# Performance work log

Hardware: AMD Instinct MI355X
Metric: run time of the kernel (lower is better)

Reference implementation:

```python
import jax, jax.numpy as jnp
import numpy as np

DIM = 512
HEADS = 8
DH = DIM // HEADS          # 64, dim_head = dim // 8
M = DIM // 2               # 256 landmarks
ITERS = 6                  # pinv iterations
KS = 33                    # residual depthwise conv kernel (lucidrains default)
N_LAYERS = 2
LN_EPS = 1e-5


def layer_norm(x, scale, bias):
    mu = x.mean(-1, keepdims=True)
    var = ((x - mu) ** 2).mean(-1, keepdims=True)
    return (x - mu) * jax.lax.rsqrt(var + LN_EPS) * scale + bias


def sinusoidal_pe(T, d, dtype):
    pos = np.arange(T)[:, None]
    div = np.exp(np.arange(0, d, 2) * (-np.log(10000.0) / d))
    pe = np.zeros((T, d), dtype=np.float32)
    pe[:, 0::2] = np.sin(pos * div)
    pe[:, 1::2] = np.cos(pos * div)
    return jnp.asarray(pe, dtype=dtype)


def iter_pinv(x):
    # Newton-Schulz Moore-Penrose iteration (lucidrains), global-max scaling
    ax = jnp.abs(x)
    denom = ax.sum(-1).max() * ax.sum(-2).max()
    z = jnp.swapaxes(x, -1, -2) / denom
    I = jnp.eye(x.shape[-1], dtype=x.dtype)
    for _ in range(ITERS):
        xz = x @ z
        z = 0.25 * (z @ (13.0 * I - xz @ (15.0 * I - xz @ (7.0 * I - xz))))
    return z


def nystrom_attention(x, qkv_w, out_w, out_b, conv_w):
    b, n, d = x.shape
    pad = (-n) % M                       # left-pad so seq divisible by M
    xp = jnp.pad(x, ((0, 0), (pad, 0), (0, 0)))
    N = n + pad
    q, k, v = [t.reshape(b, N, HEADS, DH).transpose(0, 2, 1, 3)
               for t in jnp.split(xp @ qkv_w, 3, axis=-1)]  # each [b,h,N,dh]
    q = q * (DH ** -0.5)
    l = N // M                           # segment length per landmark
    q_l = q.reshape(b, HEADS, M, l, DH).mean(3)   # [b,h,M,dh]
    k_l = k.reshape(b, HEADS, M, l, DH).mean(3)
    attn1 = jax.nn.softmax(jnp.einsum('bhid,bhjd->bhij', q, k_l), -1)    # [b,h,N,M]
    attn2 = jax.nn.softmax(jnp.einsum('bhid,bhjd->bhij', q_l, k_l), -1)  # [b,h,M,M]
    attn3 = jax.nn.softmax(jnp.einsum('bhid,bhjd->bhij', q_l, k), -1)    # [b,h,M,N]
    out = attn1 @ (iter_pinv(attn2) @ (attn3 @ v))                       # [b,h,N,dh]
    # residual depthwise conv over sequence, per head (groups=heads)
    P = KS // 2
    out = out + jax.lax.conv_general_dilated(
        v, conv_w, (1, 1), ((P, P), (0, 0)),
        dimension_numbers=('NCHW', 'OIHW', 'NCHW'), feature_group_count=HEADS)
    out = out.transpose(0, 2, 1, 3).reshape(b, N, d)
    out = out @ out_w + out_b
    return out[:, -n:]


def setup_inputs() -> dict:
    key = jax.random.key(0)
    ks = jax.random.split(key, 12)
    B, T, IN_DIM = 4, 4095, 1024
    s = 0.02
    return {
        'data': jax.random.normal(ks[0], (B, T, IN_DIM), jnp.float32),
        'fc1_w': jax.random.normal(ks[1], (IN_DIM, DIM), jnp.float32) * s,
        'fc1_b': jnp.zeros((DIM,), jnp.float32),
        'cls_token': jax.random.normal(ks[2], (1, 1, DIM), jnp.float32),
        'ln_scale': jnp.ones((N_LAYERS, DIM), jnp.float32),
        'ln_bias': jnp.zeros((N_LAYERS, DIM), jnp.float32),
        'qkv_w': jax.random.normal(ks[3], (N_LAYERS, DIM, 3 * DIM), jnp.float32) * s,
        'out_w': jax.random.normal(ks[4], (N_LAYERS, DIM, DIM), jnp.float32) * s,
        'out_b': jnp.zeros((N_LAYERS, DIM), jnp.float32),
        'conv_w': jax.random.normal(ks[5], (N_LAYERS, HEADS, 1, KS, 1), jnp.float32) * s,
        'fnorm_scale': jnp.ones((DIM,), jnp.float32),
        'fnorm_bias': jnp.zeros((DIM,), jnp.float32),
        'fcout_w': jax.random.normal(ks[6], (DIM, 1), jnp.float32) * s,
        'fcout_b': jnp.zeros((1,), jnp.float32),
    }


def reference(data, fc1_w, fc1_b, cls_token, ln_scale, ln_bias, qkv_w, out_w,
              out_b, conv_w, fnorm_scale, fnorm_bias, fcout_w, fcout_b):
    B, T, _ = data.shape
    h = jax.nn.relu(data @ fc1_w + fc1_b)
    h = h + sinusoidal_pe(T, DIM, h.dtype)
    cls = jnp.broadcast_to(cls_token, (B, 1, DIM))
    h = jnp.concatenate([cls, h], axis=1)
    for i in range(N_LAYERS):
        h = h + nystrom_attention(layer_norm(h, ln_scale[i], ln_bias[i]),
                                  qkv_w[i], out_w[i], out_b[i], conv_w[i])
    h = layer_norm(h, fnorm_scale, fnorm_bias)
    logits = (h[:, 0] @ fcout_w + fcout_b)[:, 0]
    y_prob = jax.nn.sigmoid(logits)
    y_hat = (y_prob > 0.5).astype(jnp.int32)
    return logits, y_prob, y_hat
```

## Files before the change

### kernel.cpp

```cpp
#include <hip/hip_runtime.h>
#include <math.h>

typedef long long ll;
typedef __attribute__((ext_vector_type(8))) short short8;
typedef __attribute__((ext_vector_type(4))) float f32x4;

#define NBATCH 4
#define TSEQ   4095
#define NTOK   4096
#define DMODEL 512
#define NHEAD  8
#define DHEAD  64
#define NLAND  256
#define INDIM  1024
#define KCONV  33
#define NBH    32
#define NSPLIT 8

__device__ __forceinline__ float bred(float* red, float v, int tid, int op){
  red[tid] = v; __syncthreads();
  for (int s = 128; s > 0; s >>= 1){
    if (tid < s) red[tid] = op ? fmaxf(red[tid], red[tid+s]) : (red[tid] + red[tid+s]);
    __syncthreads();
  }
  float r = red[0];
  __syncthreads();
  return r;
}

__device__ __forceinline__ short f2bf(float f){
  unsigned u = __float_as_uint(f);
  u += 0x7fff + ((u>>16)&1);
  return (short)(u>>16);
}
__device__ __forceinline__ float bf2f(short s){
  return __uint_as_float(((unsigned)(unsigned short)s) << 16);
}

__global__ __launch_bounds__(256) void pe_table_k(float* __restrict__ pe){
  int idx = blockIdx.x*256 + threadIdx.x;
  if (idx >= TSEQ*DMODEL) return;
  int c = idx & 511; int t = idx >> 9;
  const double NEG = -9.210340371976184 / 512.0;
  double div = exp((double)(c & ~1) * NEG);
  float ang = (float)((double)t * div);
  pe[idx] = (c & 1) ? cosf(ang) : sinf(ang);
}

__global__ __launch_bounds__(256) void pe_cls_add_k(float* __restrict__ hb, const float* __restrict__ cls,
                                                    const float* __restrict__ pe){
  ll idx = (ll)blockIdx.x*256 + threadIdx.x;
  int c = (int)(idx & 511);
  ll rn = idx >> 9;
  int n = (int)(rn & 4095);
  if (n == 0) hb[idx] = cls[c];
  else        hb[idx] += pe[(ll)(n-1)*512 + c];
}

__global__ __launch_bounds__(256) void cvt_bf16_k(const float* __restrict__ in, short* __restrict__ out, int n8){
  int idx = blockIdx.x*256 + threadIdx.x;
  for (int i = idx; i < n8; i += gridDim.x*256){
    const f32x4* p = (const f32x4*)(in + (ll)i*8);
    f32x4 a = p[0], b = p[1];
    short8 v;
    v[0]=f2bf(a[0]); v[1]=f2bf(a[1]); v[2]=f2bf(a[2]); v[3]=f2bf(a[3]);
    v[4]=f2bf(b[0]); v[5]=f2bf(b[1]); v[6]=f2bf(b[2]); v[7]=f2bf(b[3]);
    ((short8*)out)[i] = v;
  }
}

__global__ __launch_bounds__(256) void transpose_bf16_k(const float* __restrict__ in, short* __restrict__ out,
                                                        int K, int N, ll sIn, ll sOut){
  __shared__ float t[64][65];
  int L = blockIdx.z;
  in  += (ll)L*sIn;
  out += (ll)L*sOut;
  int n0 = blockIdx.x*64, k0 = blockIdx.y*64;
  int tid = threadIdx.x;
  for (int e = tid; e < 4096; e += 256){
    int r = e >> 6, c = e & 63;
    t[r][c] = in[(ll)(k0 + r)*N + n0 + c];
  }
  __syncthreads();
  for (int e = tid; e < 4096; e += 256){
    int r = e >> 6, c = e & 63;
    out[(ll)(n0 + r)*K + k0 + c] = f2bf(t[c][r]);
  }
}

__global__ __launch_bounds__(256) void ln_rows_k(const float* __restrict__ in, short* __restrict__ out,
                                                 const float* __restrict__ sc, const float* __restrict__ bi){
  __shared__ float red[256];
  ll row = blockIdx.x;
  const float* xr = in + row*DMODEL;
  short* orow = out + row*DMODEL;
  int tid = threadIdx.x;
  float v0 = xr[tid], v1 = xr[tid+256];
  float mu = bred(red, v0+v1, tid, 0) * (1.f/512.f);
  float d0 = v0-mu, d1 = v1-mu;
  float var = bred(red, d0*d0 + d1*d1, tid, 0) * (1.f/512.f);
  float inv = 1.f / sqrtf(var + 1e-5f);
  orow[tid]     = f2bf(d0*inv*sc[tid]     + bi[tid]);
  orow[tid+256] = f2bf(d1*inv*sc[tid+256] + bi[tid+256]);
}

template<int BM, int BN, int AB, int BMODE, int CB, int SW>
__global__ __launch_bounds__(256)
void mgemm(const void* __restrict__ Av, const void* __restrict__ Bv,
           void* __restrict__ Cv, const void* __restrict__ Ev,
           const float* __restrict__ bias,
           int Mr, int K, int lda, int ldb, int ldc,
           ll sA, ll sB, ll sC,
           float c0, float c1, int flags)
{
  constexpr int MI = BM/32, NJ = BN/32;
  __shared__ __align__(16) short As[BM*64];
  __shared__ __align__(16) short Bs[BN*64];
  int z = blockIdx.z;
  int bx = blockIdx.x, by = blockIdx.y;
  if (SW){
    int nwg = gridDim.x*gridDim.y;
    int lin = by*gridDim.x + bx;
    int q = nwg >> 3, r = nwg & 7;
    int xcd = lin & 7, idx = lin >> 3;
    int wg = (xcd < r) ? (xcd*(q+1) + idx) : (r*(q+1) + (xcd - r)*q + idx);
    bx = wg % gridDim.x; by = wg / gridDim.x;
  }
  int n0 = bx*BN, m0 = by*BM;
  int tid = threadIdx.x;
  int lane = tid & 63, w = tid >> 6;
  int wr = w >> 1, wc = w & 1;
  int l15 = lane & 15, l4 = lane >> 4;

  f32x4 acc[MI][NJ];
  #pragma unroll
  for (int i = 0; i < MI; i++)
    #pragma unroll
    for (int j = 0; j < NJ; j++) acc[i][j] = (f32x4){0.f,0.f,0.f,0.f};

  for (int k0 = 0; k0 < K; k0 += 64){
    #pragma unroll
    for (int it = 0; it < BM/32; ++it){
      int tau = tid + 256*it;
      int row = tau >> 3, slot = tau & 7;
      int grow = m0 + row;
      short8 v;
      if (AB){
        if (grow < Mr) v = *(const short8*)((const short*)Av + (ll)z*sA + (ll)grow*lda + k0 + slot*8);
        else v = (short8){0,0,0,0,0,0,0,0};
      } else {
        f32x4 p0 = {0.f,0.f,0.f,0.f}, p1 = {0.f,0.f,0.f,0.f};
        if (grow < Mr){
          const float* ap = (const float*)Av + (ll)z*sA + (ll)grow*lda + k0 + slot*8;
          p0 = *(const f32x4*)ap; p1 = *(const f32x4*)(ap+4);
        }
        v[0]=f2bf(p0[0]); v[1]=f2bf(p0[1]); v[2]=f2bf(p0[2]); v[3]=f2bf(p0[3]);
        v[4]=f2bf(p1[0]); v[5]=f2bf(p1[1]); v[6]=f2bf(p1[2]); v[7]=f2bf(p1[3]);
      }
      ((short8*)As)[row*8 + (slot ^ (row&7))] = v;
    }
    #pragma unroll
    for (int it = 0; it < BN/32; ++it){
      int tau = tid + 256*it;
      if (BMODE == 2){
        int n = tau >> 3, slot = tau & 7;
        short8 v = *(const short8*)((const short*)Bv + (ll)z*sB + (ll)(n0 + n)*ldb + k0 + slot*8);
        ((short8*)Bs)[n*8 + (slot ^ (n&7))] = v;
      } else {
        int n = tau & (BN-1), slot = tau >> (BN==128 ? 7 : 6);
        short8 v;
        if (BMODE == 1){
          const short* bp = (const short*)Bv + (ll)z*sB + (ll)(k0 + slot*8)*ldb + n0 + n;
          #pragma unroll
          for (int i = 0; i < 8; i++) v[i] = bp[(ll)i*ldb];
        } else {
          const float* bp = (const float*)Bv + (ll)z*sB + (ll)(k0 + slot*8)*ldb + n0 + n;
          #pragma unroll
          for (int i = 0; i < 8; i++) v[i] = f2bf(bp[(ll)i*ldb]);
        }
        ((short8*)Bs)[n*8 + (slot ^ (n&7))] = v;
      }
    }
    __syncthreads();
    #pragma unroll
    for (int kc = 0; kc < 2; kc++){
      short8 af[MI], bfr[NJ];
      #pragma unroll
      for (int i = 0; i < MI; i++){
        int row = wr*(BM/2) + i*16 + l15;
        int g = kc*4 + l4;
        af[i] = ((short8*)As)[row*8 + (g ^ (row&7))];
      }
      #pragma unroll
      for (int j = 0; j < NJ; j++){
        int col = wc*(BN/2) + j*16 + l15;
        int g = kc*4 + l4;
        bfr[j] = ((short8*)Bs)[col*8 + (g ^ (col&7))];
      }
      #pragma unroll
      for (int i = 0; i < MI; i++)
        #pragma unroll
        for (int j = 0; j < NJ; j++)
          acc[i][j] = __builtin_amdgcn_mfma_f32_16x16x32_bf16(af[i], bfr[j], acc[i][j], 0, 0, 0);
    }
    __syncthreads();
  }

  #pragma unroll
  for (int i = 0; i < MI; i++){
    int rbase = m0 + wr*(BM/2) + i*16 + l4*4;
    #pragma unroll
    for (int j = 0; j < NJ; j++){
      int col = n0 + wc*(BN/2) + j*16 + l15;
      #pragma unroll
      for (int r = 0; r < 4; r++){
        int m = rbase + r;
        if (m >= Mr) continue;
        float v = acc[i][j][r];
        if (flags & 4){
          float ev = CB ? bf2f(((const short*)Ev + (ll)z*sC)[(ll)m*ldc + col])
                        : ((const float*)Ev + (ll)z*sC)[(ll)m*ldc + col];
          v = c0 * ev + c1 * v;
        }
        if (flags & 1) v += bias[col];
        if (flags & 2) v = fmaxf(v, 0.f);
        int om = (flags & 16) ? (m + m/TSEQ + 1) : m;
        ll ci = (ll)z*sC + (ll)om*ldc + col;
        if (CB){
          short* Cs = (short*)Cv;
          if (flags & 8) v += bf2f(Cs[ci]);
          Cs[ci] = f2bf(v);
        } else {
          float* Cf = (float*)Cv;
          if (flags & 8) v += Cf[ci];
          Cf[ci] = v;
        }
      }
    }
  }
}

__global__ __launch_bounds__(256)
void gemm_nt(const short* __restrict__ A, const short* __restrict__ Bm, float* __restrict__ C,
             int lda, int ldb, int ldc,
             ll sAb, ll sAh, ll sBb, ll sBh, ll sCb, ll sCh,
             float alpha)
{
  __shared__ float As[64][65];
  __shared__ float Bs[64][65];
  int z = blockIdx.z; int b = z >> 3; int h = z & 7;
  A  += (ll)b*sAb + (ll)h*sAh;
  Bm += (ll)b*sBb + (ll)h*sBh;
  C  += (ll)b*sCb + (ll)h*sCh;
  int n0 = blockIdx.x*64, m0 = blockIdx.y*64;
  int tid = threadIdx.x;
  int kk = tid & 63, rr = tid >> 6;
  #pragma unroll
  for (int r = 0; r < 16; r++){
    As[rr + 4*r][kk] = bf2f(A [(ll)(m0 + rr + 4*r)*lda + kk]);
    Bs[rr + 4*r][kk] = bf2f(Bm[(ll)(n0 + rr + 4*r)*ldb + kk]);
  }
  __syncthreads();
  int tx = tid & 15, ty = tid >> 4;
  float acc[4][4] = {};
  for (int k = 0; k < 64; k++){
    float a[4], bv[4];
    #pragma unroll
    for (int i = 0; i < 4; i++) a[i] = As[ty + 16*i][k];
    #pragma unroll
    for (int j = 0; j < 4; j++) bv[j] = Bs[tx + 16*j][k];
    #pragma unroll
    for (int i = 0; i < 4; i++)
      #pragma unroll
      for (int j = 0; j < 4; j++)
        acc[i][j] += a[i]*bv[j];
  }
  #pragma unroll
  for (int i = 0; i < 4; i++)
    #pragma unroll
    for (int j = 0; j < 4; j++)
      C[(ll)(m0 + ty + 16*i)*ldc + n0 + tx + 16*j] = alpha * acc[i][j];
}

__global__ __launch_bounds__(256)
void mflash_k(const short* __restrict__ Q, const short* __restrict__ K,
              const short* __restrict__ V, short* __restrict__ O,
              int ldq, int ldk, int ldv, int ldo, int nkeys, float alpha,
              ll sQb, ll sQh, ll sKb, ll sKh, ll sVb, ll sVh, ll sOb, ll sOh)
{
  __shared__ __align__(16) short Qs[64*64];
  __shared__ __align__(16) short Ks[64*64];
  __shared__ __align__(16) short Vs[64*64];
  __shared__ __align__(16) short Ps[64*64];
  __shared__ float Sl[64][68];
  __shared__ float m_l[64], s_l[64], scl[64];
  int z = blockIdx.z; int b = z >> 3; int h = z & 7;
  Q += (ll)b*sQb + (ll)h*sQh;
  K += (ll)b*sKb + (ll)h*sKh;
  V += (ll)b*sVb + (ll)h*sVh;
  O += (ll)b*sOb + (ll)h*sOh;
  int m0 = blockIdx.x*64;
  int tid = threadIdx.x;
  int lane = tid & 63, w = tid >> 6;
  int l15 = lane & 15, l4 = lane >> 4;
  int wr = w >> 1, wc = w & 1;

  #pragma unroll
  for (int it = 0; it < 2; it++){
    int tau = tid + 256*it;
    int row = tau >> 3, slot = tau & 7;
    short8 v = *(const short8*)(Q + (ll)(m0 + row)*ldq + slot*8);
    ((short8*)Qs)[row*8 + (slot ^ (row&7))] = v;
  }
  if (tid < 64){ m_l[tid] = -1e30f; s_l[tid] = 0.f; }
  f32x4 o[2][2];
  #pragma unroll
  for (int i = 0; i < 2; i++)
    #pragma unroll
    for (int j = 0; j < 2; j++) o[i][j] = (f32x4){0.f,0.f,0.f,0.f};

  for (int n0 = 0; n0 < nkeys; n0 += 64){
// ... 208 lines not shown
    for (int i = 0; i < 2; i++)
      #pragma unroll
      for (int j = 0; j < 2; j++)
        #pragma unroll
        for (int r = 0; r < 4; r++)
          Sl[wr*32 + i*16 + l4*4 + r][wc*32 + j*16 + l15] = s[i][j][r];
    __syncthreads();
    {
      int row = tid >> 2, q = tid & 3, cb = q*16;
      float sv[16];
      float cmax = -1e30f;
      #pragma unroll
      for (int cc = 0; cc < 16; cc++){ sv[cc] = Sl[row][cb+cc]; cmax = fmaxf(cmax, sv[cc]); }
      cmax = fmaxf(cmax, __shfl_xor(cmax, 1));
      cmax = fmaxf(cmax, __shfl_xor(cmax, 2));
      float mprev = m_l[row];
      float newm = fmaxf(mprev, cmax);
      float lsum = 0.f;
      short8 pv0, pv1;
      #pragma unroll
      for (int cc = 0; cc < 8; cc++){ float e = expf(sv[cc]-newm); lsum += e; pv0[cc] = f2bf(e); }
      #pragma unroll
      for (int cc = 0; cc < 8; cc++){ float e = expf(sv[8+cc]-newm); lsum += e; pv1[cc] = f2bf(e); }
      lsum += __shfl_xor(lsum, 1);
      lsum += __shfl_xor(lsum, 2);
      ((short8*)Ps)[row*8 + ((2*q)   ^ (row&7))] = pv0;
      ((short8*)Ps)[row*8 + ((2*q+1) ^ (row&7))] = pv1;
      if (q == 0){
        float scale = expf(mprev - newm);
        m_l[row] = newm;
        s_l[row] = s_l[row]*scale + lsum;
        scl[row] = scale;
      }
    }
    __syncthreads();
    #pragma unroll
    for (int i = 0; i < 2; i++)
      #pragma unroll
      for (int r = 0; r < 4; r++){
        float sc = scl[wr*32 + i*16 + l4*4 + r];
        #pragma unroll
        for (int j = 0; j < 2; j++) o[i][j][r] *= sc;
      }
    #pragma unroll
    for (int kc = 0; kc < 2; kc++){
      short8 ap[2], bv[2];
      int g = kc*4 + l4;
      #pragma unroll
      for (int i = 0; i < 2; i++){
        int row = wr*32 + i*16 + l15;
        ap[i] = ((short8*)Ps)[row*8 + (g ^ (row&7))];
      }
      #pragma unroll
      for (int j = 0; j < 2; j++){
        int d = wc*32 + j*16 + l15;
        bv[j] = ((short8*)Vs)[d*8 + (g ^ (d&7))];
      }
      #pragma unroll
      for (int i = 0; i < 2; i++)
        #pragma unroll
        for (int j = 0; j < 2; j++)
          o[i][j] = __builtin_amdgcn_mfma_f32_16x16x32_bf16(ap[i], bv[j], o[i][j], 0, 0, 0);
    }
  }
  int bs = z*NSPLIT + split;
  #pragma unroll
  for (int i = 0; i < 2; i++)
    #pragma unroll
    for (int j = 0; j < 2; j++)
      #pragma unroll
      for (int r = 0; r < 4; r++){
        int row = wr*32 + i*16 + l4*4 + r;
        int col = wc*32 + j*16 + l15;
        po[((ll)bs*NLAND + m0 + row)*64 + col] = o[i][j][r];
      }
  if (tid < 64){
    pm[(ll)bs*NLAND + m0 + tid] = m_l[tid];
    pl[(ll)bs*NLAND + m0 + tid] = s_l[tid];
  }
}

__global__ __launch_bounds__(256)
void flash3_comb_k(const float* __restrict__ po, const float* __restrict__ pm,
                   const float* __restrict__ pl, short* __restrict__ av){
  int bh = blockIdx.y;
  int row = blockIdx.x*4 + (threadIdx.x >> 6);
  int col = threadIdx.x & 63;
  float ms = -1e30f;
  float mv[NSPLIT];
  #pragma unroll
  for (int s = 0; s < NSPLIT; s++){
    mv[s] = pm[((ll)bh*NSPLIT + s)*NLAND + row];
    ms = fmaxf(ms, mv[s]);
  }
  float osum = 0.f, lsum = 0.f;
  #pragma unroll
  for (int s = 0; s < NSPLIT; s++){
    float wgt = expf(mv[s] - ms);
    osum += wgt * po[(((ll)bh*NSPLIT + s)*NLAND + row)*64 + col];
    lsum += wgt * pl[((ll)bh*NSPLIT + s)*NLAND + row];
  }
  av[((ll)bh*NLAND + row)*64 + col] = f2bf(osum / lsum);
}

__global__ __launch_bounds__(256) void softmax_rows_k(float* __restrict__ data, short* __restrict__ out16,
                                                      int cols){
  __shared__ float red[256];
  float* row = data + (ll)blockIdx.x * cols;
  short* row16 = out16 ? out16 + (ll)blockIdx.x * cols : nullptr;
  int tid = threadIdx.x;
  float m = -1e30f;
  for (int c = tid; c < cols; c += 256) m = fmaxf(m, row[c]);
  m = bred(red, m, tid, 1);
  float s = 0.f;
  for (int c = tid; c < cols; c += 256){ float e = expf(row[c] - m); row[c] = e; s += e; }
  s = bred(red, s, tid, 0);
  float inv = 1.f/s;
  for (int c = tid; c < cols; c += 256){
    float p = row[c] * inv;
    row[c] = p;
    if (row16) row16[c] = f2bf(p);
  }
}

__global__ __launch_bounds__(256) void landmarks_k(const short* __restrict__ qkv,
                                                   short* __restrict__ ql, short* __restrict__ kl){
  int idx = blockIdx.x*256 + threadIdx.x;
  int d = idx & 63;
  int i = (idx >> 6) & 255;
  int h = (idx >> 14) & 7;
  int b = idx >> 17;
  const short* base = qkv + ((ll)b*NTOK + (ll)i*16)*1536 + h*64 + d;
  float sq = 0.f, sk = 0.f;
  #pragma unroll
  for (int l = 0; l < 16; l++){ sq += bf2f(base[l*1536]); sk += bf2f(base[l*1536 + 512]); }
  ql[idx] = f2bf(sq * (0.125f/16.f));
  kl[idx] = f2bf(sk * (1.f/16.f));
}

__global__ void init_scal_k(unsigned* s){ s[0] = 0u; s[1] = 0u; }

__global__ __launch_bounds__(256) void a2_maxsums_k(const float* __restrict__ a2, unsigned* __restrict__ gm){
  __shared__ float red[256];
  const float* A = a2 + (ll)blockIdx.x*65536;
  int tid = threadIdx.x;
  float cs = 0.f, rs = 0.f;
  for (int i = 0; i < 256; i++) cs += A[i*256 + tid];
  for (int j = 0; j < 256; j++) rs += A[tid*256 + j];
  float cmax = bred(red, cs, tid, 1);
  float rmax = bred(red, rs, tid, 1);
  if (tid == 0){
    atomicMax(gm + 0, __float_as_uint(rmax));
    atomicMax(gm + 1, __float_as_uint(cmax));
  }
}

__global__ __launch_bounds__(256) void zinit_k(const float* __restrict__ a2, short* __restrict__ z,
                                               const unsigned* __restrict__ gm){
  float inv = 1.f / (__uint_as_float(gm[0]) * __uint_as_float(gm[1]));
  int idx = blockIdx.x*256 + threadIdx.x;
  int j = idx & 255, i = (idx >> 8) & 255, bh = idx >> 16;
  z[idx] = f2bf(a2[(ll)bh*65536 + j*256 + i] * inv);
}

__global__ __launch_bounds__(256) void dwconv_add_k(const short* __restrict__ qkv,
                                                    const float* __restrict__ cw, short* __restrict__ out){
  __shared__ float sv[160][64];
  __shared__ float w[KCONV];
  int z = blockIdx.y; int b = z >> 3; int h = z & 7;
  int t0 = blockIdx.x * 128;
  int tid = threadIdx.x;
  if (tid < KCONV) w[tid] = cw[h*KCONV + tid];
  const short* vbase = qkv + (ll)b*NTOK*1536 + 1024 + h*64;
  for (int e = tid; e < 160*64; e += 256){
    int r = e >> 6, d = e & 63;
    int t = t0 - 16 + r;
    sv[r][d] = (t >= 0 && t < NTOK) ? bf2f(vbase[(ll)t*1536 + d]) : 0.f;
  }
  __syncthreads();
  short* obase = out + (ll)b*NTOK*512 + h*64;
  for (int e = tid; e < 128*64; e += 256){
    int r = e >> 6, d = e & 63;
    float s = 0.f;
    #pragma unroll
    for (int kk = 0; kk < KCONV; kk++) s += sv[r+kk][d]*w[kk];
    ll oi = (ll)(t0+r)*512 + d;
    obase[oi] = f2bf(bf2f(obase[oi]) + s);
  }
}

__global__ __launch_bounds__(256) void head_k(const float* __restrict__ hb, const float* __restrict__ fns,
      const float* __restrict__ fnb, const float* __restrict__ fw, const float* __restrict__ fb,
      float* __restrict__ out){
  __shared__ float red[256];
  int b = blockIdx.x;
  const float* xr = hb + (ll)b*NTOK*DMODEL;
  int tid = threadIdx.x;
  float v0 = xr[tid], v1 = xr[tid+256];
  float mu = bred(red, v0+v1, tid, 0) * (1.f/512.f);
  float d0 = v0-mu, d1 = v1-mu;
  float var = bred(red, d0*d0 + d1*d1, tid, 0) * (1.f/512.f);
  float inv = 1.f/sqrtf(var + 1e-5f);
  float y0 = d0*inv*fns[tid]     + fnb[tid];
  float y1 = d1*inv*fns[tid+256] + fnb[tid+256];
  float dot = bred(red, y0*fw[tid] + y1*fw[tid+256], tid, 0);
  if (tid == 0){
    float logit = dot + fb[0];
    float prob = 1.f/(1.f + expf(-logit));
    out[b] = logit; out[4+b] = prob; out[8+b] = (prob > 0.5f) ? 1.f : 0.f;
  }
}

extern "C" void kernel_launch(void* const* d_in, const int* in_sizes, int n_in,
                              void* d_out, int out_size, void* d_ws, size_t ws_size,
                              hipStream_t stream)
{
  (void)in_sizes; (void)n_in; (void)out_size;
  const float* data  = (const float*)d_in[0];
  const float* fc1_w = (const float*)d_in[1];
  const float* fc1_b = (const float*)d_in[2];
  const float* cls   = (const float*)d_in[3];
  const float* ln_s  = (const float*)d_in[4];
  const float* ln_b  = (const float*)d_in[5];
  const float* qkv_w = (const float*)d_in[6];
  const float* out_w = (const float*)d_in[7];
  const float* out_b = (const float*)d_in[8];
  const float* convw = (const float*)d_in[9];
  const float* fns   = (const float*)d_in[10];
  const float* fnb   = (const float*)d_in[11];
  const float* fcw   = (const float*)d_in[12];
  const float* fcb   = (const float*)d_in[13];
  float* out = (float*)d_out;
  float* ws  = (float*)d_ws;

  float* h    = ws;
  short* xb   = (short*)(h + 8388608);
  short* qkvh = xb + 8388608;
  short* ql   = qkvh + 25165824;
  short* kl   = ql + 524288;
  float* a2f  = (float*)(kl + 524288);
  short* a2h  = (short*)(a2f + 2097152);
  short* zA   = a2h + 2097152;
  short* zB   = zA + 2097152;
  short* t1   = zB + 2097152;
  short* t2   = t1 + 2097152;
  short* t3   = t2 + 2097152;
  short* av   = t3 + 2097152;
  short* y2   = av + 524288;
  float* po   = (float*)(y2 + 524288);
  float* pm   = po + 4194304;
  float* pl   = pm + 65536;
  float* pe   = pl + 65536;
  short* datab = (short*)(pe + 2097152);
  short* fc1t  = datab + 16777216;
  short* qkvt  = fc1t + 524288;
  short* outt  = qkvt + 1572864;
  unsigned* scal = (unsigned*)(outt + 524288);

  const size_t NEED = (size_t)((char*)(scal + 2) - (char*)ws);
  if (ws_size < NEED) return;

  pe_table_k<<<(TSEQ*DMODEL + 255)/256, 256, 0, stream>>>(pe);
  cvt_bf16_k<<<2048, 256, 0, stream>>>(data, datab, (NBATCH*TSEQ*INDIM)/8);
  transpose_bf16_k<<<dim3(8, 16, 1), 256, 0, stream>>>(fc1_w, fc1t, INDIM, DMODEL, 0, 0);
  transpose_bf16_k<<<dim3(24, 8, 2), 256, 0, stream>>>(qkv_w, qkvt, DMODEL, 1536,
                                                       (ll)DMODEL*1536, (ll)1536*DMODEL);
  transpose_bf16_k<<<dim3(8, 8, 2), 256, 0, stream>>>(out_w, outt, DMODEL, DMODEL,
                                                      (ll)DMODEL*DMODEL, (ll)DMODEL*DMODEL);

  mgemm<128,128,1,2,0,1><<<dim3(4, 128, 1), 256, 0, stream>>>(
      datab, fc1t, h, nullptr, fc1_b,
      NBATCH*TSEQ, INDIM, INDIM, INDIM, DMODEL,
      0, 0, 0, 0.f, 0.f, 1|2|16);
  pe_cls_add_k<<<(NBATCH*NTOK*DMODEL)/256, 256, 0, stream>>>(h, cls, pe);

  for (int L = 0; L < 2; L++){
    const float* ob = out_b + (ll)L*DMODEL;
    const float* cw = convw + (ll)L*NHEAD*KCONV;
    const short* qwt = qkvt + (ll)L*1536*DMODEL;
    const short* owt = outt + (ll)L*DMODEL*DMODEL;

    ln_rows_k<<<NBATCH*NTOK, 256, 0, stream>>>(h, xb, ln_s + L*DMODEL, ln_b + L*DMODEL);
    mgemm<128,128,1,2,1,1><<<dim3(12, 128, 1), 256, 0, stream>>>(
        xb, qwt, qkvh, nullptr, nullptr,
        NBATCH*NTOK, DMODEL, DMODEL, DMODEL, 1536,
        0, 0, 0, 0.f, 0.f, 0);
    landmarks_k<<<2048, 256, 0, stream>>>(qkvh, ql, kl);

    gemm_nt<<<dim3(4, 4, NBH), 256, 0, stream>>>(
        ql, kl, a2f, 64, 64, 256,
        131072, 16384, 131072, 16384, 524288, 65536, 1.f);
    softmax_rows_k<<<NBH*NLAND, 256, 0, stream>>>(a2f, a2h, 256);

    init_scal_k<<<1, 1, 0, stream>>>(scal);
    a2_maxsums_k<<<NBH, 256, 0, stream>>>(a2f, scal);
    zinit_k<<<8192, 256, 0, stream>>>(a2f, zA, scal);

    short* zc = zA; short* zn = zB;
    for (int it = 0; it < 6; it++){
      mgemm<64,64,1,1,1,0><<<dim3(4, 4, NBH), 256, 0, stream>>>(
          a2h, zc, t1, nullptr, nullptr, 256, 256, 256, 256, 256,
          65536, 65536, 65536, 0.f, 0.f, 0);
      mgemm<64,64,1,1,1,0><<<dim3(4, 4, NBH), 256, 0, stream>>>(
          t1, t1, t2, t1, nullptr, 256, 256, 256, 256, 256,
          65536, 65536, 65536, 7.f, -1.f, 4);
      mgemm<64,64,1,1,1,0><<<dim3(4, 4, NBH), 256, 0, stream>>>(
          t1, t2, t3, t1, nullptr, 256, 256, 256, 256, 256,
          65536, 65536, 65536, 15.f, -1.f, 4);
      mgemm<64,64,1,1,1,0><<<dim3(4, 4, NBH), 256, 0, stream>>>(
          zc, t3, zn, zc, nullptr, 256, 256, 256, 256, 256,
          65536, 65536, 65536, 3.25f, -0.25f, 4);
      short* tmp = zc; zc = zn; zn = tmp;
    }

    mflash3_part_k<<<dim3(4, NSPLIT, NBH), 256, 0, stream>>>(
        ql, qkvh + 512, qkvh + 1024, po, pm, pl,
        64, 1536, 1536,
        131072, 16384, (ll)NTOK*1536, 64, (ll)NTOK*1536, 64);
    flash3_comb_k<<<dim3(64, NBH), 256, 0, stream>>>(po, pm, pl, av);

    mgemm<64,64,1,1,1,0><<<dim3(1, 4, NBH), 256, 0, stream>>>(
        zc, av, y2, nullptr, nullptr, 256, 256, 256, 64, 64,
        65536, 16384, 16384, 0.f, 0.f, 0);

    mflash_k<<<dim3(64, 1, NBH), 256, 0, stream>>>(
        qkvh, kl, y2, xb,
        1536, 64, 64, 512, NLAND, 0.125f,
        (ll)NTOK*1536, 64, 131072, 16384, 131072, 16384, (ll)NTOK*512, 64);

    dwconv_add_k<<<dim3(32, NBH), 256, 0, stream>>>(qkvh, cw, xb);

    mgemm<128,128,1,2,0,1><<<dim3(4, 128, 1), 256, 0, stream>>>(
        xb, owt, h, nullptr, ob,
        NBATCH*NTOK, DMODEL, DMODEL, DMODEL, DMODEL,
        0, 0, 0, 0.f, 0.f, 1|8);
  }

  head_k<<<4, 256, 0, stream>>>(h, fns, fnb, fcw, fcb, out);
}
```

Baseline: 1.308 ms.

## Fuse Newton-Schulz pinv chain into one cooperative kernel with grid syncs

Replaces the zinit kernel, the 24 small batched GEMM launches of the pseudo-inverse iteration and the final z@av GEMM with one cooperative kernel of 512 blocks. Each block owns a 64x64 tile of one head and uses grid.sync between dependent GEMM stages. The goal is to remove per-launch overhead and tail gaps across roughly 26 kernels per layer. The risks are the cost of the grid-wide barriers, a new and possibly slower inline GEMM tile with strided scalar B loads, and a fallback path if cooperative launch fails.

```diff
diff --git a/kernel.cpp b/kernel.cpp
--- a/kernel.cpp
+++ b/kernel.cpp
@@ -1,5 +1,8 @@
 #include <hip/hip_runtime.h>
+#include <hip/hip_cooperative_groups.h>
 #include <math.h>
+
+namespace cg = cooperative_groups;
 
 typedef long long ll;
 typedef __attribute__((ext_vector_type(8))) short short8;
@@ -237,6 +240,126 @@
         }
       }
     }
+  }
+}
+
+__device__ __forceinline__ void gtile(const short* __restrict__ A, int lda,
+                                      const short* __restrict__ B, int ldb,
+                                      short* __restrict__ C, int ldc,
+                                      const short* __restrict__ E, int lde,
+                                      int Kdim, float c0, float c1,
+                                      int m0, int n0, int tid,
+                                      short* As, short* Bs)
+{
+  int lane = tid & 63, w = tid >> 6;
+  int wr = w >> 1, wc = w & 1;
+  int l15 = lane & 15, l4 = lane >> 4;
+  f32x4 acc[2][2];
+  #pragma unroll
+  for (int i = 0; i < 2; i++)
+    #pragma unroll
+    for (int j = 0; j < 2; j++) acc[i][j] = (f32x4){0.f,0.f,0.f,0.f};
+
+  for (int k0 = 0; k0 < Kdim; k0 += 64){
+    __syncthreads();
+    #pragma unroll
+    for (int it = 0; it < 2; ++it){
+      int tau = tid + 256*it;
+      int row = tau >> 3, slot = tau & 7;
+      short8 v = *(const short8*)(A + (ll)(m0 + row)*lda + k0 + slot*8);
+      ((short8*)As)[row*8 + (slot ^ (row&7))] = v;
+    }
+    #pragma unroll
+    for (int it = 0; it < 2; ++it){
+      int tau = tid + 256*it;
+      int n = tau & 63, slot = tau >> 6;
+      const short* bp = B + (ll)(k0 + slot*8)*ldb + n0 + n;
+      short8 v;
+      #pragma unroll
+      for (int i = 0; i < 8; i++) v[i] = bp[(ll)i*ldb];
+      ((short8*)Bs)[n*8 + (slot ^ (n&7))] = v;
+    }
+    __syncthreads();
+    #pragma unroll
+    for (int kc = 0; kc < 2; kc++){
+      short8 af[2], bfr[2];
+      int g = kc*4 + l4;
+      #pragma unroll
+      for (int i = 0; i < 2; i++){
+        int row = i*16 + wr*32 + l15;
+        af[i] = ((short8*)As)[row*8 + (g ^ (row&7))];
+      }
+      #pragma unroll
+      for (int j = 0; j < 2; j++){
+        int col = j*16 + wc*32 + l15;
+        bfr[j] = ((short8*)Bs)[col*8 + (g ^ (col&7))];
+      }
+      #pragma unroll
+      for (int i = 0; i < 2; i++)
+        #pragma unroll
+        for (int j = 0; j < 2; j++)
+          acc[i][j] = __builtin_amdgcn_mfma_f32_16x16x32_bf16(af[i], bfr[j], acc[i][j], 0, 0, 0);
+    }
+  }
+  #pragma unroll
+  for (int i = 0; i < 2; i++)
+    #pragma unroll
+    for (int j = 0; j < 2; j++)
+      #pragma unroll
+      for (int r = 0; r < 4; r++){
+        int row = m0 + wr*32 + i*16 + l4*4 + r;
+        int col = n0 + wc*32 + j*16 + l15;
+        float v = c1 * acc[i][j][r];
+        if (E) v += c0 * bf2f(E[(ll)row*lde + col]);
+        C[(ll)row*ldc + col] = f2bf(v);
+      }
+}
+
+__global__ __launch_bounds__(256)
+void pinv_chain_k(const float* __restrict__ a2f, const short* __restrict__ a2h,
+                  short* __restrict__ zAg, short* __restrict__ zBg,
+                  short* __restrict__ t1g, short* __restrict__ t2g, short* __restrict__ t3g,
+                  const short* __restrict__ avg, short* __restrict__ y2g,
+                  const unsigned* __restrict__ gm)
+{
+  __shared__ __align__(16) short As[64*64];
+  __shared__ __align__(16) short Bs[64*64];
+  cg::grid_group grid = cg::this_grid();
+  int blk = blockIdx.x;
+  int bh = blk >> 4, tile = blk & 15;
+  int m0 = (tile >> 2)*64, n0 = (tile & 3)*64;
+  int tid = threadIdx.x;
+  const float* a2F = a2f + (ll)bh*65536;
+  const short* a2H = a2h + (ll)bh*65536;
+  short* zA = zAg + (ll)bh*65536;
+  short* zB = zBg + (ll)bh*65536;
+  short* t1 = t1g + (ll)bh*65536;
+  short* t2 = t2g + (ll)bh*65536;
+  short* t3 = t3g + (ll)bh*65536;
+
+  float inv = 1.f / (__uint_as_float(gm[0]) * __uint_as_float(gm[1]));
+  for (int e = tid; e < 4096; e += 256){
+    int r = e >> 6, c = e & 63;
+    zA[(ll)(m0 + r)*256 + n0 + c] = f2bf(a2F[(ll)(n0 + c)*256 + m0 + r] * inv);
+  }
+  grid.sync();
+
+  short* zc = zA; short* zn = zB;
+  for (int it = 0; it < 6; it++){
+    gtile(a2H, 256, zc, 256, t1, 256, nullptr, 256, 256, 0.f, 1.f, m0, n0, tid, As, Bs);
+    grid.sync();
+    gtile(t1, 256, t1, 256, t2, 256, t1, 256, 256, 7.f, -1.f, m0, n0, tid, As, Bs);
+    grid.sync();
+    gtile(t1, 256, t2, 256, t3, 256, t1, 256, 256, 15.f, -1.f, m0, n0, tid, As, Bs);
+    grid.sync();
+    gtile(zc, 256, t3, 256, zn, 256, zc, 256, 256, 3.25f, -0.25f, m0, n0, tid, As, Bs);
+    grid.sync();
+    short* tmp = zc; zc = zn; zn = tmp;
+  }
+  if ((tile & 3) == 0){
+    const short* av = avg + (ll)bh*16384;
+    short* y2 = y2g + (ll)bh*16384;
+    gtile(zc, 256, av, 64, y2, 64, nullptr, 64, 256, 0.f, 1.f, m0, 0, tid, As, Bs);
   }
 }
 
@@ -820,27 +943,8 @@
         ql, kl, a2f, 64, 64, 256,
         131072, 16384, 131072, 16384, 524288, 65536, 1.f);
     softmax_rows_k<<<NBH*NLAND, 256, 0, stream>>>(a2f, a2h, 256);
-
     init_scal_k<<<1, 1, 0, stream>>>(scal);
     a2_maxsums_k<<<NBH, 256, 0, stream>>>(a2f, scal);
-    zinit_k<<<8192, 256, 0, stream>>>(a2f, zA, scal);
-
-    short* zc = zA; short* zn = zB;
-    for (int it = 0; it < 6; it++){
-      mgemm<64,64,1,1,1,0><<<dim3(4, 4, NBH), 256, 0, stream>>>(
-          a2h, zc, t1, nullptr, nullptr, 256, 256, 256, 256, 256,
-          65536, 65536, 65536, 0.f, 0.f, 0);
-      mgemm<64,64,1,1,1,0><<<dim3(4, 4, NBH), 256, 0, stream>>>(
-          t1, t1, t2, t1, nullptr, 256, 256, 256, 256, 256,
-          65536, 65536, 65536, 7.f, -1.f, 4);
-      mgemm<64,64,1,1,1,0><<<dim3(4, 4, NBH), 256, 0, stream>>>(
-          t1, t2, t3, t1, nullptr, 256, 256, 256, 256, 256,
-          65536, 65536, 65536, 15.f, -1.f, 4);
-      mgemm<64,64,1,1,1,0><<<dim3(4, 4, NBH), 256, 0, stream>>>(
-          zc, t3, zn, zc, nullptr, 256, 256, 256, 256, 256,
-          65536, 65536, 65536, 3.25f, -0.25f, 4);
-      short* tmp = zc; zc = zn; zn = tmp;
-    }
 
     mflash3_part_k<<<dim3(4, NSPLIT, NBH), 256, 0, stream>>>(
         ql, qkvh + 512, qkvh + 1024, po, pm, pl,
@@ -848,9 +952,35 @@
         131072, 16384, (ll)NTOK*1536, 64, (ll)NTOK*1536, 64);
     flash3_comb_k<<<dim3(64, NBH), 256, 0, stream>>>(po, pm, pl, av);
 
-    mgemm<64,64,1,1,1,0><<<dim3(1, 4, NBH), 256, 0, stream>>>(
-        zc, av, y2, nullptr, nullptr, 256, 256, 256, 64, 64,
-        65536, 16384, 16384, 0.f, 0.f, 0);
+    {
+      void* args[] = { (void*)&a2f, (void*)&a2h, (void*)&zA, (void*)&zB,
+                       (void*)&t1, (void*)&t2, (void*)&t3,
+                       (void*)&av, (void*)&y2, (void*)&scal };
+      hipError_t e = hipLaunchCooperativeKernel((void*)pinv_chain_k,
+                                                dim3(512), dim3(256), args, 0, stream);
+      if (e != hipSuccess){
+        zinit_k<<<8192, 256, 0, stream>>>(a2f, zA, scal);
+        short* zc = zA; short* zn = zB;
+        for (int it = 0; it < 6; it++){
+          mgemm<64,64,1,1,1,0><<<dim3(4, 4, NBH), 256, 0, stream>>>(
+              a2h, zc, t1, nullptr, nullptr, 256, 256, 256, 256, 256,
+              65536, 65536, 65536, 0.f, 0.f, 0);
+          mgemm<64,64,1,1,1,0><<<dim3(4, 4, NBH), 256, 0, stream>>>(
+              t1, t1, t2, t1, nullptr, 256, 256, 256, 256, 256,
+              65536, 65536, 65536, 7.f, -1.f, 4);
+          mgemm<64,64,1,1,1,0><<<dim3(4, 4, NBH), 256, 0, stream>>>(
+              t1, t2, t3, t1, nullptr, 256, 256, 256, 256, 256,
+              65536, 65536, 65536, 15.f, -1.f, 4);
+          mgemm<64,64,1,1,1,0><<<dim3(4, 4, NBH), 256, 0, stream>>>(
+              zc, t3, zn, zc, nullptr, 256, 256, 256, 256, 256,
+              65536, 65536, 65536, 3.25f, -0.25f, 4);
+          short* tmp = zc; zc = zn; zn = tmp;
+        }
+        mgemm<64,64,1,1,1,0><<<dim3(1, 4, NBH), 256, 0, stream>>>(
+            zc, av, y2, nullptr, nullptr, 256, 256, 256, 64, 64,
+            65536, 16384, 16384, 0.f, 0.f, 0);
+      }
+    }
 
     mflash_k<<<dim3(64, 1, NBH), 256, 0, stream>>>(
         qkvh, kl, y2, xb,
```

Result: slower. 3.931 ms (+200.6%).

## Use direct global-to-LDS loads and transposed operands in pinv GEMM chain

Applied to the files above, without the earlier changes.

The GEMM tile loaders now use global_load_lds to copy bf16 A and B tiles straight into shared memory when rows are in bounds, skipping the register staging step. The Newton-Schulz pinv GEMMs and the final z·av GEMM switch from strided column-gathered B loads (BMODE 1) to row-contiguous loads of transposed operands. Each epilogue therefore also writes a transposed bf16 copy, and the z init and attention-combine kernels emit transposed buffers too. This trades extra scattered transposed stores and workspace aliasing (reusing datab) for vectorized B loads.

```diff
diff --git a/kernel.cpp b/kernel.cpp
--- a/kernel.cpp
+++ b/kernel.cpp
@@ -35,6 +35,11 @@
 }
 __device__ __forceinline__ float bf2f(short s){
   return __uint_as_float(((unsigned)(unsigned short)s) << 16);
+}
+
+__device__ __forceinline__ void gload16(const void* g, void* l){
+  __builtin_amdgcn_global_load_lds((const __attribute__((address_space(1))) void*)g,
+                                   (__attribute__((address_space(3))) void*)l, 16, 0, 0);
 }
 
 __global__ __launch_bounds__(256) void pe_table_k(float* __restrict__ pe){
@@ -107,7 +112,7 @@
 template<int BM, int BN, int AB, int BMODE, int CB, int SW>
 __global__ __launch_bounds__(256)
 void mgemm(const void* __restrict__ Av, const void* __restrict__ Bv,
-           void* __restrict__ Cv, const void* __restrict__ Ev,
+           void* __restrict__ Cv, const void* __restrict__ Ev, void* __restrict__ CTv,
            const float* __restrict__ bias,
            int Mr, int K, int lda, int ldb, int ldc,
            ll sA, ll sB, ll sC,
@@ -131,6 +136,7 @@
   int lane = tid & 63, w = tid >> 6;
   int wr = w >> 1, wc = w & 1;
   int l15 = lane & 15, l4 = lane >> 4;
+  bool fullM = (m0 + BM <= Mr);
 
   f32x4 acc[MI][NJ];
   #pragma unroll
@@ -139,34 +145,50 @@
     for (int j = 0; j < NJ; j++) acc[i][j] = (f32x4){0.f,0.f,0.f,0.f};
 
   for (int k0 = 0; k0 < K; k0 += 64){
-    #pragma unroll
-    for (int it = 0; it < BM/32; ++it){
-      int tau = tid + 256*it;
-      int row = tau >> 3, slot = tau & 7;
-      int grow = m0 + row;
-      short8 v;
-      if (AB){
-        if (grow < Mr) v = *(const short8*)((const short*)Av + (ll)z*sA + (ll)grow*lda + k0 + slot*8);
-        else v = (short8){0,0,0,0,0,0,0,0};
-      } else {
-        f32x4 p0 = {0.f,0.f,0.f,0.f}, p1 = {0.f,0.f,0.f,0.f};
-        if (grow < Mr){
-          const float* ap = (const float*)Av + (ll)z*sA + (ll)grow*lda + k0 + slot*8;
-          p0 = *(const f32x4*)ap; p1 = *(const f32x4*)(ap+4);
+    if (AB && fullM){
+      #pragma unroll
+      for (int it = 0; it < BM/32; ++it){
+        int base = (w*(BM/32) + it)*64;
+        int ls = base + lane;
+        int row = ls >> 3, slot = ls & 7;
+        const short* gp = (const short*)Av + (ll)z*sA + (ll)(m0 + row)*lda + k0 + ((slot ^ (row&7))<<3);
+        gload16(gp, (char*)As + (ll)base*16);
+      }
+    } else {
+      #pragma unroll
+      for (int it = 0; it < BM/32; ++it){
+        int tau = tid + 256*it;
+        int row = tau >> 3, slot = tau & 7;
+        int grow = m0 + row;
+        short8 v;
+        if (AB){
+          if (grow < Mr) v = *(const short8*)((const short*)Av + (ll)z*sA + (ll)grow*lda + k0 + slot*8);
+          else v = (short8){0,0,0,0,0,0,0,0};
+        } else {
+          f32x4 p0 = {0.f,0.f,0.f,0.f}, p1 = {0.f,0.f,0.f,0.f};
+          if (grow < Mr){
+            const float* ap = (const float*)Av + (ll)z*sA + (ll)grow*lda + k0 + slot*8;
+            p0 = *(const f32x4*)ap; p1 = *(const f32x4*)(ap+4);
+          }
+          v[0]=f2bf(p0[0]); v[1]=f2bf(p0[1]); v[2]=f2bf(p0[2]); v[3]=f2bf(p0[3]);
+          v[4]=f2bf(p1[0]); v[5]=f2bf(p1[1]); v[6]=f2bf(p1[2]); v[7]=f2bf(p1[3]);
         }
-        v[0]=f2bf(p0[0]); v[1]=f2bf(p0[1]); v[2]=f2bf(p0[2]); v[3]=f2bf(p0[3]);
-        v[4]=f2bf(p1[0]); v[5]=f2bf(p1[1]); v[6]=f2bf(p1[2]); v[7]=f2bf(p1[3]);
-      }
-      ((short8*)As)[row*8 + (slot ^ (row&7))] = v;
-    }
-    #pragma unroll
-    for (int it = 0; it < BN/32; ++it){
-      int tau = tid + 256*it;
-      if (BMODE == 2){
-        int n = tau >> 3, slot = tau & 7;
-        short8 v = *(const short8*)((const short*)Bv + (ll)z*sB + (ll)(n0 + n)*ldb + k0 + slot*8);
-        ((short8*)Bs)[n*8 + (slot ^ (n&7))] = v;
-      } else {
+        ((short8*)As)[row*8 + (slot ^ (row&7))] = v;
+      }
+    }
+    if (BMODE == 2){
+      #pragma unroll
+      for (int it = 0; it < BN/32; ++it){
+        int base = (w*(BN/32) + it)*64;
+        int ls = base + lane;
+        int n = ls >> 3, slot = ls & 7;
+        const short* gp = (const short*)Bv + (ll)z*sB + (ll)(n0 + n)*ldb + k0 + ((slot ^ (n&7))<<3);
+        gload16(gp, (char*)Bs + (ll)base*16);
+      }
+    } else {
+      #pragma unroll
+      for (int it = 0; it < BN/32; ++it){
+        int tau = tid + 256*it;
         int n = tau & (BN-1), slot = tau >> (BN==128 ? 7 : 6);
         short8 v;
         if (BMODE == 1){
@@ -235,6 +257,8 @@
           if (flags & 8) v += Cf[ci];
           Cf[ci] = v;
         }
+        if (flags & 32)
+          ((short*)CTv)[(ll)z*sC + (ll)col*256 + m] = f2bf(v);
       }
     }
   }
@@ -611,7 +635,7 @@
 
 __global__ __launch_bounds__(256)
 void flash3_comb_k(const float* __restrict__ po, const float* __restrict__ pm,
-                   const float* __restrict__ pl, short* __restrict__ av){
+                   const float* __restrict__ pl, short* __restrict__ av, short* __restrict__ avT){
   int bh = blockIdx.y;
   int row = blockIdx.x*4 + (threadIdx.x >> 6);
   int col = threadIdx.x & 63;
@@ -629,7 +653,9 @@
     osum += wgt * po[(((ll)bh*NSPLIT + s)*NLAND + row)*64 + col];
     lsum += wgt * pl[((ll)bh*NSPLIT + s)*NLAND + row];
   }
-  av[((ll)bh*NLAND + row)*64 + col] = f2bf(osum / lsum);
+  short r = f2bf(osum / lsum);
+  av [((ll)bh*NLAND + row)*64 + col] = r;
+  avT[(ll)bh*16384 + (ll)col*256 + row] = r;
 }
 
 __global__ __launch_bounds__(256) void softmax_rows_k(float* __restrict__ data, short* __restrict__ out16,
@@ -685,11 +711,12 @@
 }
 
 __global__ __launch_bounds__(256) void zinit_k(const float* __restrict__ a2, short* __restrict__ z,
-                                               const unsigned* __restrict__ gm){
+                                               short* __restrict__ zT, const unsigned* __restrict__ gm){
   float inv = 1.f / (__uint_as_float(gm[0]) * __uint_as_float(gm[1]));
   int idx = blockIdx.x*256 + threadIdx.x;
   int j = idx & 255, i = (idx >> 8) & 255, bh = idx >> 16;
-  z[idx] = f2bf(a2[(ll)bh*65536 + j*256 + i] * inv);
+  z [idx] = f2bf(a2[(ll)bh*65536 + j*256 + i] * inv);
+  zT[idx] = f2bf(a2[idx] * inv);
 }
 
 __global__ __launch_bounds__(256) void dwconv_add_k(const short* __restrict__ qkv,
@@ -785,6 +812,12 @@
   short* qkvt  = fc1t + 524288;
   short* outt  = qkvt + 1572864;
   unsigned* scal = (unsigned*)(outt + 524288);
+  short* zAT = datab;
+  short* zBT = zAT + 2097152;
+  short* t1T = zBT + 2097152;
+  short* t2T = t1T + 2097152;
+  short* t3T = t2T + 2097152;
+  short* avT = t3T + 2097152;
 
   const size_t NEED = (size_t)((char*)(scal + 2) - (char*)ws);
   if (ws_size < NEED) return;
@@ -798,7 +831,7 @@
                                                       (ll)DMODEL*DMODEL, (ll)DMODEL*DMODEL);
 
   mgemm<128,128,1,2,0,1><<<dim3(4, 128, 1), 256, 0, stream>>>(
-      datab, fc1t, h, nullptr, fc1_b,
+      datab, fc1t, h, nullptr, nullptr, fc1_b,
       NBATCH*TSEQ, INDIM, INDIM, INDIM, DMODEL,
       0, 0, 0, 0.f, 0.f, 1|2|16);
   pe_cls_add_k<<<(NBATCH*NTOK*DMODEL)/256, 256, 0, stream>>>(h, cls, pe);
@@ -811,7 +844,7 @@
 
     ln_rows_k<<<NBATCH*NTOK, 256, 0, stream>>>(h, xb, ln_s + L*DMODEL, ln_b + L*DMODEL);
     mgemm<128,128,1,2,1,1><<<dim3(12, 128, 1), 256, 0, stream>>>(
-        xb, qwt, qkvh, nullptr, nullptr,
+        xb, qwt, qkvh, nullptr, nullptr, nullptr,
         NBATCH*NTOK, DMODEL, DMODEL, DMODEL, 1536,
         0, 0, 0, 0.f, 0.f, 0);
     landmarks_k<<<2048, 256, 0, stream>>>(qkvh, ql, kl);
@@ -820,37 +853,37 @@
         ql, kl, a2f, 64, 64, 256,
         131072, 16384, 131072, 16384, 524288, 65536, 1.f);
     softmax_rows_k<<<NBH*NLAND, 256, 0, stream>>>(a2f, a2h, 256);
-
     init_scal_k<<<1, 1, 0, stream>>>(scal);
     a2_maxsums_k<<<NBH, 256, 0, stream>>>(a2f, scal);
-    zinit_k<<<8192, 256, 0, stream>>>(a2f, zA, scal);
-
-    short* zc = zA; short* zn = zB;
-    for (int it = 0; it < 6; it++){
-      mgemm<64,64,1,1,1,0><<<dim3(4, 4, NBH), 256, 0, stream>>>(
-          a2h, zc, t1, nullptr, nullptr, 256, 256, 256, 256, 256,
-          65536, 65536, 65536, 0.f, 0.f, 0);
-      mgemm<64,64,1,1,1,0><<<dim3(4, 4, NBH), 256, 0, stream>>>(
-          t1, t1, t2, t1, nullptr, 256, 256, 256, 256, 256,
-          65536, 65536, 65536, 7.f, -1.f, 4);
-      mgemm<64,64,1,1,1,0><<<dim3(4, 4, NBH), 256, 0, stream>>>(
-          t1, t2, t3, t1, nullptr, 256, 256, 256, 256, 256,
-          65536, 65536, 65536, 15.f, -1.f, 4);
-      mgemm<64,64,1,1,1,0><<<dim3(4, 4, NBH), 256, 0, stream>>>(
-          zc, t3, zn, zc, nullptr, 256, 256, 256, 256, 256,
-          65536, 65536, 65536, 3.25f, -0.25f, 4);
-      short* tmp = zc; zc = zn; zn = tmp;
-    }
 
     mflash3_part_k<<<dim3(4, NSPLIT, NBH), 256, 0, stream>>>(
         ql, qkvh + 512, qkvh + 1024, po, pm, pl,
         64, 1536, 1536,
         131072, 16384, (ll)NTOK*1536, 64, (ll)NTOK*1536, 64);
-    flash3_comb_k<<<dim3(64, NBH), 256, 0, stream>>>(po, pm, pl, av);
-
-    mgemm<64,64,1,1,1,0><<<dim3(1, 4, NBH), 256, 0, stream>>>(
-        zc, av, y2, nullptr, nullptr, 256, 256, 256, 64, 64,
-        65536, 16384, 16384, 0.f, 0.f, 0);
+    flash3_comb_k<<<dim3(64, NBH), 256, 0, stream>>>(po, pm, pl, av, avT);
+
+    zinit_k<<<8192, 256, 0, stream>>>(a2f, zA, zAT, scal);
+    short *zc = zA, *zcT = zAT, *zn = zB, *znT = zBT;
+    for (int it = 0; it < 6; it++){
+      mgemm<64,64,1,2,1,0><<<dim3(4, 4, NBH), 256, 0, stream>>>(
+          a2h, zcT, t1, nullptr, t1T, nullptr, 256, 256, 256, 256, 256,
+          65536, 65536, 65536, 0.f, 1.f, 32);
+      mgemm<64,64,1,2,1,0><<<dim3(4, 4, NBH), 256, 0, stream>>>(
+          t1, t1T, t2, t1, t2T, nullptr, 256, 256, 256, 256, 256,
+          65536, 65536, 65536, 7.f, -1.f, 4|32);
+      mgemm<64,64,1,2,1,0><<<dim3(4, 4, NBH), 256, 0, stream>>>(
+          t1, t2T, t3, t1, t3T, nullptr, 256, 256, 256, 256, 256,
+          65536, 65536, 65536, 15.f, -1.f, 4|32);
+      mgemm<64,64,1,2,1,0><<<dim3(4, 4, NBH), 256, 0, stream>>>(
+          zc, t3T, zn, zc, znT, nullptr, 256, 256, 256, 256, 256,
+          65536, 65536, 65536, 3.25f, -0.25f, 4|32);
+      short* s;
+      s = zc; zc = zn; zn = s;
+      s = zcT; zcT = znT; znT = s;
+    }
+    mgemm<64,64,1,2,1,0><<<dim3(1, 4, NBH), 256, 0, stream>>>(
+        zc, avT, y2, nullptr, nullptr, nullptr, 256, 256, 256, 256, 64,
+        65536, 16384, 16384, 0.f, 1.f, 0);
 
     mflash_k<<<dim3(64, 1, NBH), 256, 0, stream>>>(
         qkvh, kl, y2, xb,
@@ -860,7 +893,7 @@
     dwconv_add_k<<<dim3(32, NBH), 256, 0, stream>>>(qkvh, cw, xb);
 
     mgemm<128,128,1,2,0,1><<<dim3(4, 128, 1), 256, 0, stream>>>(
-        xb, owt, h, nullptr, ob,
+        xb, owt, h, nullptr, nullptr, ob,
         NBATCH*NTOK, DMODEL, DMODEL, DMODEL, DMODEL,
         0, 0, 0, 0.f, 0.f, 1|8);
   }
```

Result: slower. 1.391 ms (+6.4%).

## Use direct global-to-LDS loads in GEMM tiles and register-block depthwise conv

Applied to the files above, without the earlier changes.

The bf16 GEMM tile loaders for A (when the tile is fully in range) and for row-major B now use global_load_lds. This copies 16-byte chunks straight into shared memory with the XOR swizzle folded into the source address, skipping the round trip through registers. Separately, the depthwise conv kernel loads V with vectorized 16-byte reads, holds the weights in registers, and has each thread slide a 64-element register window over 32 outputs, which cuts LDS traffic. The cost is higher register pressure in the conv kernel and a dependency on the async LDS-load builtin behaving correctly.

```diff
diff --git a/kernel.cpp b/kernel.cpp
--- a/kernel.cpp
+++ b/kernel.cpp
@@ -35,6 +35,11 @@
 }
 __device__ __forceinline__ float bf2f(short s){
   return __uint_as_float(((unsigned)(unsigned short)s) << 16);
+}
+
+__device__ __forceinline__ void gload16(const void* g, void* l){
+  __builtin_amdgcn_global_load_lds((const __attribute__((address_space(1))) void*)g,
+                                   (__attribute__((address_space(3))) void*)l, 16, 0, 0);
 }
 
 __global__ __launch_bounds__(256) void pe_table_k(float* __restrict__ pe){
@@ -131,6 +136,7 @@
   int lane = tid & 63, w = tid >> 6;
   int wr = w >> 1, wc = w & 1;
   int l15 = lane & 15, l4 = lane >> 4;
+  bool fullM = (m0 + BM <= Mr);
 
   f32x4 acc[MI][NJ];
   #pragma unroll
@@ -139,34 +145,50 @@
     for (int j = 0; j < NJ; j++) acc[i][j] = (f32x4){0.f,0.f,0.f,0.f};
 
   for (int k0 = 0; k0 < K; k0 += 64){
-    #pragma unroll
-    for (int it = 0; it < BM/32; ++it){
-      int tau = tid + 256*it;
-      int row = tau >> 3, slot = tau & 7;
-      int grow = m0 + row;
-      short8 v;
-      if (AB){
-        if (grow < Mr) v = *(const short8*)((const short*)Av + (ll)z*sA + (ll)grow*lda + k0 + slot*8);
-        else v = (short8){0,0,0,0,0,0,0,0};
-      } else {
-        f32x4 p0 = {0.f,0.f,0.f,0.f}, p1 = {0.f,0.f,0.f,0.f};
-        if (grow < Mr){
-          const float* ap = (const float*)Av + (ll)z*sA + (ll)grow*lda + k0 + slot*8;
-          p0 = *(const f32x4*)ap; p1 = *(const f32x4*)(ap+4);
+    if (AB && fullM){
+      #pragma unroll
+      for (int it = 0; it < BM/32; ++it){
+        int base = (w*(BM/32) + it)*64;
+        int ls = base + lane;
+        int row = ls >> 3, slot = ls & 7;
+        const short* gp = (const short*)Av + (ll)z*sA + (ll)(m0 + row)*lda + k0 + ((slot ^ (row&7))<<3);
+        gload16(gp, (char*)As + (ll)base*16);
+      }
+    } else {
+      #pragma unroll
+      for (int it = 0; it < BM/32; ++it){
+        int tau = tid + 256*it;
+        int row = tau >> 3, slot = tau & 7;
+        int grow = m0 + row;
+        short8 v;
+        if (AB){
+          if (grow < Mr) v = *(const short8*)((const short*)Av + (ll)z*sA + (ll)grow*lda + k0 + slot*8);
+          else v = (short8){0,0,0,0,0,0,0,0};
+        } else {
+          f32x4 p0 = {0.f,0.f,0.f,0.f}, p1 = {0.f,0.f,0.f,0.f};
+          if (grow < Mr){
+            const float* ap = (const float*)Av + (ll)z*sA + (ll)grow*lda + k0 + slot*8;
+            p0 = *(const f32x4*)ap; p1 = *(const f32x4*)(ap+4);
+          }
+          v[0]=f2bf(p0[0]); v[1]=f2bf(p0[1]); v[2]=f2bf(p0[2]); v[3]=f2bf(p0[3]);
+          v[4]=f2bf(p1[0]); v[5]=f2bf(p1[1]); v[6]=f2bf(p1[2]); v[7]=f2bf(p1[3]);
         }
-        v[0]=f2bf(p0[0]); v[1]=f2bf(p0[1]); v[2]=f2bf(p0[2]); v[3]=f2bf(p0[3]);
-        v[4]=f2bf(p1[0]); v[5]=f2bf(p1[1]); v[6]=f2bf(p1[2]); v[7]=f2bf(p1[3]);
-      }
-      ((short8*)As)[row*8 + (slot ^ (row&7))] = v;
-    }
-    #pragma unroll
-    for (int it = 0; it < BN/32; ++it){
-      int tau = tid + 256*it;
-      if (BMODE == 2){
-        int n = tau >> 3, slot = tau & 7;
-        short8 v = *(const short8*)((const short*)Bv + (ll)z*sB + (ll)(n0 + n)*ldb + k0 + slot*8);
-        ((short8*)Bs)[n*8 + (slot ^ (n&7))] = v;
-      } else {
+        ((short8*)As)[row*8 + (slot ^ (row&7))] = v;
+      }
+    }
+    if (BMODE == 2){
+      #pragma unroll
+      for (int it = 0; it < BN/32; ++it){
+        int base = (w*(BN/32) + it)*64;
+        int ls = base + lane;
+        int n = ls >> 3, slot = ls & 7;
+        const short* gp = (const short*)Bv + (ll)z*sB + (ll)(n0 + n)*ldb + k0 + ((slot ^ (n&7))<<3);
+        gload16(gp, (char*)Bs + (ll)base*16);
+      }
+    } else {
+      #pragma unroll
+      for (int it = 0; it < BN/32; ++it){
+        int tau = tid + 256*it;
         int n = tau & (BN-1), slot = tau >> (BN==128 ? 7 : 6);
         short8 v;
         if (BMODE == 1){
@@ -695,25 +717,33 @@
 __global__ __launch_bounds__(256) void dwconv_add_k(const short* __restrict__ qkv,
                                                     const float* __restrict__ cw, short* __restrict__ out){
   __shared__ float sv[160][64];
-  __shared__ float w[KCONV];
   int z = blockIdx.y; int b = z >> 3; int h = z & 7;
   int t0 = blockIdx.x * 128;
   int tid = threadIdx.x;
-  if (tid < KCONV) w[tid] = cw[h*KCONV + tid];
   const short* vbase = qkv + (ll)b*NTOK*1536 + 1024 + h*64;
-  for (int e = tid; e < 160*64; e += 256){
-    int r = e >> 6, d = e & 63;
+  for (int e8 = tid; e8 < 1280; e8 += 256){
+    int r = e8 >> 3, d8 = (e8 & 7)*8;
     int t = t0 - 16 + r;
-    sv[r][d] = (t >= 0 && t < NTOK) ? bf2f(vbase[(ll)t*1536 + d]) : 0.f;
-  }
+    short8 v = (t >= 0 && t < NTOK) ? *(const short8*)(vbase + (ll)t*1536 + d8)
+                                    : (short8){0,0,0,0,0,0,0,0};
+    #pragma unroll
+    for (int j = 0; j < 8; j++) sv[r][d8 + j] = bf2f(v[j]);
+  }
+  float wreg[KCONV];
+  #pragma unroll
+  for (int kk = 0; kk < KCONV; kk++) wreg[kk] = cw[h*KCONV + kk];
   __syncthreads();
-  short* obase = out + (ll)b*NTOK*512 + h*64;
-  for (int e = tid; e < 128*64; e += 256){
-    int r = e >> 6, d = e & 63;
+  int d = tid & 63, g = tid >> 6;
+  float vals[64];
+  #pragma unroll
+  for (int j = 0; j < 64; j++) vals[j] = sv[g*32 + j][d];
+  short* obase = out + (ll)b*NTOK*512 + h*64 + d;
+  #pragma unroll
+  for (int t = 0; t < 32; t++){
     float s = 0.f;
     #pragma unroll
-    for (int kk = 0; kk < KCONV; kk++) s += sv[r+kk][d]*w[kk];
-    ll oi = (ll)(t0+r)*512 + d;
+    for (int kk = 0; kk < KCONV; kk++) s += vals[t + kk]*wreg[kk];
+    ll oi = (ll)(t0 + g*32 + t)*512;
     obase[oi] = f2bf(bf2f(obase[oi]) + s);
   }
 }
@@ -820,7 +850,6 @@
         ql, kl, a2f, 64, 64, 256,
         131072, 16384, 131072, 16384, 524288, 65536, 1.f);
     softmax_rows_k<<<NBH*NLAND, 256, 0, stream>>>(a2f, a2h, 256);
-
     init_scal_k<<<1, 1, 0, stream>>>(scal);
     a2_maxsums_k<<<NBH, 256, 0, stream>>>(a2f, scal);
     zinit_k<<<8192, 256, 0, stream>>>(a2f, zA, scal);
```

Measured after the change: 1.141 ms. 1.15x faster.
